# Optimization experiments

Hardware: AMD Instinct MI355X
Metric: run time of the kernel (lower is better)

Reference implementation:

```python
import math
import jax, jax.numpy as jnp
import numpy as np


def _unskew(X):
    # X: B x M x (M+L)  ->  B x M x L (each row i shifted left by i)
    B, M, MpL = X.shape
    L = MpL - M
    X = X.reshape(B, M * MpL)
    X = jnp.pad(X, ((0, 0), (0, M)))          # B x (M*(M+L)+M)
    X = X.reshape(B, M, MpL + 1)               # B x M x (M+L+1)
    return X[:, :, :L]


def _skew(X, pad_value):
    # X: B x M x L  ->  B x M x (M+L) (each row i shifted right by i)
    B, M, L = X.shape
    X = jnp.pad(X, ((0, 0), (0, 0), (0, M + 1)), constant_values=pad_value)
    X = X.reshape(B, -1)[:, :-M]               # B x (M*(M+L))
    return X.reshape(B, M, M + L)


def setup_inputs() -> dict:
    key = jax.random.key(0)
    k1, k2, k3, k4 = jax.random.split(key, 4)
    B, M, L, H = 128, 512, 1024, 64   # B = batch*heads, key len = M+L
    query = jax.random.normal(k1, (B, M, H), dtype=jnp.float32)
    key_t = jax.random.normal(k2, (B, M + L, H), dtype=jnp.float32)
    value = jax.random.normal(k3, (B, M + L, H), dtype=jnp.float32)
    key_pe = jax.random.normal(k4, (1, H, L), dtype=jnp.float32) * 0.02
    return {"query": query, "key": key_t, "value": value, "key_pe": key_pe}


def reference(query, key, value, key_pe):
    H = query.shape[-1]  # head_dim
    # content attention: B x M x (M+L), then unskew to relative coords B x M x L
    attn_cont = jnp.einsum('bmh,bnh->bmn', query, key)
    attn_cont = _unskew(attn_cont)
    # position attention: B x M x L (key_pe broadcasts over batch)
    attn_pos = jnp.einsum('bmh,xhl->bml', query, key_pe)
    attn = (attn_cont + attn_pos) / math.sqrt(H)
    attn = jax.nn.softmax(attn, axis=-1)
    # dropout p=0.0 -> identity
    attn_sk = _skew(attn, 0.0)                  # B x M x (M+L)
    out = jnp.einsum('bmn,bnh->bmh', attn_sk, value)
    return out
```

## Files before the change

kernel.cpp:

```cpp
#include <hip/hip_runtime.h>
#include <math.h>

typedef __bf16 bf16x8 __attribute__((ext_vector_type(8)));
typedef __bf16 bf16x4 __attribute__((ext_vector_type(4)));
typedef float  f32x4  __attribute__((ext_vector_type(4)));

constexpr int B_  = 128;
constexpr int M_  = 512;
constexpr int L_  = 1024;
constexpr int H_  = 64;
constexpr int KL_ = 1536;

constexpr int BM = 64;
constexpr int KT = 64;
constexpr int NT = 17;
constexpr int KS = 72;
constexpr int PPS = 256;
constexpr int PSS = 40;

constexpr int OFF_KS   = 0;
constexpr int OFF_VT   = 18432;
constexpr int OFF_PPOS = 36864;
constexpr int OFF_PS   = 69632;
constexpr int SMEM_BYTES = 79872;
constexpr int OFF_OBUF = 0;
constexpr int OFF_LSUM = 18432;
constexpr int OBS = 36;

#define MFMA16(A, B, C) __builtin_amdgcn_mfma_f32_16x16x32_bf16((A), (B), (C), 0, 0, 0)

__global__ __launch_bounds__(256, 2)
void seqattn_v5(const float* __restrict__ Q, const float* __restrict__ K,
                const float* __restrict__ V, const float* __restrict__ PE,
                float* __restrict__ O) {
  __shared__ alignas(16) char smem[SMEM_BYTES];
  __bf16* ksb  = (__bf16*)(smem + OFF_KS);
  __bf16* vtb  = (__bf16*)(smem + OFF_VT);
  __bf16* ppos = (__bf16*)(smem + OFF_PPOS);

  const int tid  = threadIdx.x;
  const int w    = tid >> 6;
  const int lane = tid & 63;
  const int nid  = lane & 15;
  const int qid  = lane >> 4;
  const int a    = w >> 1;
  const int c    = w & 1;
  const int b    = blockIdx.x;
  const int m0   = blockIdx.y * BM;
  const int swz  = qid << 4;

  __bf16* ps = (__bf16*)(smem + OFF_PS) + w * 32 * PSS;

  bf16x8 aq[2][2];
  #pragma unroll
  for (int it = 0; it < 2; ++it) {
    const float* qg = &Q[((size_t)b * M_ + m0 + 32 * a + 16 * it + nid) * H_];
    #pragma unroll
    for (int j = 0; j < 8; ++j) {
      aq[it][0][j] = (__bf16)qg[8 * qid + j];
      aq[it][1][j] = (__bf16)qg[32 + 8 * qid + j];
    }
  }

  f32x4 o[2][4];
  float lpart[2][4];
  #pragma unroll
  for (int it = 0; it < 2; ++it) {
    #pragma unroll
    for (int ht = 0; ht < 4; ++ht) o[it][ht] = (f32x4){0.f, 0.f, 0.f, 0.f};
    #pragma unroll
    for (int r = 0; r < 4; ++r) lpart[it][r] = 0.f;
  }

  const int krow = tid >> 2,  khq = (tid & 3) * 16;
  const int vj = (tid & 15) * 4, vh = (tid >> 4) * 4;

  const float* peg = &PE[(size_t)(8 * qid) * L_ + 32 * c + nid];

  f32x4 kr[4], vr[4];
  {
    const float* kg = &K[((size_t)b * KL_ + m0 + krow) * H_ + khq];
    kr[0] = *(const f32x4*)kg;       kr[1] = *(const f32x4*)(kg + 4);
    kr[2] = *(const f32x4*)(kg + 8); kr[3] = *(const f32x4*)(kg + 12);
    const float* vg = &V[((size_t)b * KL_ + m0 + vj) * H_ + vh];
    #pragma unroll
    for (int e = 0; e < 4; ++e) vr[e] = *(const f32x4*)(vg + e * H_);
  }
  {
    const f32x4 z = {0.f, 0.f, 0.f, 0.f};
    #pragma unroll
    for (int nt = 0; nt < 2; ++nt) {
      bf16x8 b0, b1;
      #pragma unroll
      for (int j = 0; j < 8; ++j) {
        b0[j] = (__bf16)peg[(size_t)j * L_ + 16 * nt];
        b1[j] = (__bf16)peg[(size_t)(32 + j) * L_ + 16 * nt];
      }
      const int colb = 32 * c + 16 * nt + nid;
      #pragma unroll
      for (int it = 0; it < 2; ++it) {
        f32x4 pp = MFMA16(aq[it][0], b0, z);
        pp = MFMA16(aq[it][1], b1, pp);
        #pragma unroll
        for (int r = 0; r < 4; ++r)
          ppos[(32 * a + 16 * it + 4 * qid + r) * PPS + (colb ^ swz)] = (__bf16)pp[r];
      }
    }
  }
  {
    bf16x8 x0, x1;
    #pragma unroll
    for (int j = 0; j < 4; ++j) {
      x0[j] = (__bf16)kr[0][j]; x0[4 + j] = (__bf16)kr[1][j];
      x1[j] = (__bf16)kr[2][j]; x1[4 + j] = (__bf16)kr[3][j];
    }
    *(bf16x8*)&ksb[krow * KS + khq] = x0;
    *(bf16x8*)&ksb[krow * KS + khq + 8] = x1;
    #pragma unroll
    for (int e = 0; e < 4; ++e) {
      bf16x4 y = {(__bf16)vr[0][e], (__bf16)vr[1][e], (__bf16)vr[2][e], (__bf16)vr[3][e]};
      *(bf16x4*)&vtb[(vh + e) * KS + vj] = y;
    }
  }
  __syncthreads();

  for (int t = 0; t < NT; ++t) {
    if (t < 16) {
      const int j1 = m0 + KT * (t + 1);
      const float* kg = &K[((size_t)b * KL_ + j1 + krow) * H_ + khq];
      kr[0] = *(const f32x4*)kg;       kr[1] = *(const f32x4*)(kg + 4);
      kr[2] = *(const f32x4*)(kg + 8); kr[3] = *(const f32x4*)(kg + 12);
      const float* vg = &V[((size_t)b * KL_ + j1 + vj) * H_ + vh];
      #pragma unroll
      for (int e = 0; e < 4; ++e) vr[e] = *(const f32x4*)(vg + e * H_);
    }
    bf16x8 pf[2][2];
    const int ch = t + 1;
    if (t < 15) {
      const float* pc = peg + ch * 64;
      #pragma unroll
      for (int nt = 0; nt < 2; ++nt) {
        #pragma unroll
        for (int j = 0; j < 8; ++j) {
          pf[nt][0][j] = (__bf16)pc[(size_t)j * L_ + 16 * nt];
          pf[nt][1][j] = (__bf16)pc[(size_t)(32 + j) * L_ + 16 * nt];
        }
      }
    }

    const __bf16* kst = ksb + (t & 1) * 64 * KS;
    const __bf16* vtt = vtb + (t & 1) * 64 * KS;
    const f32x4 z = {0.f, 0.f, 0.f, 0.f};

    f32x4 s[2][2];
    #pragma unroll
    for (int nt = 0; nt < 2; ++nt) {
      const __bf16* kb = &kst[(32 * c + 16 * nt + nid) * KS];
      const bf16x8 b0 = *(const bf16x8*)&kb[8 * qid];
      const bf16x8 b1 = *(const bf16x8*)&kb[32 + 8 * qid];
      #pragma unroll
      for (int it = 0; it < 2; ++it) {
        s[it][nt] = MFMA16(aq[it][0], b0, z);
        s[it][nt] = MFMA16(aq[it][1], b1, s[it][nt]);
      }
    }

    if (t < 15) {
      #pragma unroll
      for (int nt = 0; nt < 2; ++nt) {
        const int colb = ((ch & 3) << 6) + 32 * c + 16 * nt + nid;
        #pragma unroll
        for (int it = 0; it < 2; ++it) {
          f32x4 pp = MFMA16(aq[it][0], pf[nt][0], z);
          pp = MFMA16(aq[it][1], pf[nt][1], pp);
          #pragma unroll
          for (int r = 0; r < 4; ++r)
            ppos[(32 * a + 16 * it + 4 * qid + r) * PPS + (colb ^ swz)] = (__bf16)pp[r];
        }
      }
    }

    const bool edge = (t == 0) || (t == 16);
    #pragma unroll
    for (int it = 0; it < 2; ++it) {
      #pragma unroll
      for (int r = 0; r < 4; ++r) {
        const int il = 32 * a + 16 * it + 4 * qid + r;
        const int rb = il * PPS;
        #pragma unroll
        for (int nt = 0; nt < 2; ++nt) {
          const int l = KT * t + 32 * c + 16 * nt + nid - il;
          float p;
          if (!edge || (unsigned)l < 1024u) {
            const float pe = (float)ppos[rb + ((l & 255) ^ swz)];
            p = __expf((s[it][nt][r] + pe) * 0.125f);
          } else {
            p = 0.f;
          }
          lpart[it][r] += p;
          ps[(16 * it + 4 * qid + r) * PSS + 16 * nt + nid] = (__bf16)p;
        }
      }
    }

    #pragma unroll
    for (int it = 0; it < 2; ++it) {
      const bf16x8 ap = *(const bf16x8*)&ps[(16 * it + nid) * PSS + 8 * qid];
      #pragma unroll
      for (int ht = 0; ht < 4; ++ht) {
        o[it][ht] = MFMA16(ap, *(const bf16x8*)&vtt[(16 * ht + nid) * KS + 32 * c + 8 * qid],
                           o[it][ht]);
      }
    }

    if (t < 16) {
      __bf16* ksn = ksb + ((t + 1) & 1) * 64 * KS;
      __bf16* vtn = vtb + ((t + 1) & 1) * 64 * KS;
      bf16x8 x0, x1;
      #pragma unroll
      for (int j = 0; j < 4; ++j) {
        x0[j] = (__bf16)kr[0][j]; x0[4 + j] = (__bf16)kr[1][j];
        x1[j] = (__bf16)kr[2][j]; x1[4 + j] = (__bf16)kr[3][j];
      }
      *(bf16x8*)&ksn[krow * KS + khq] = x0;
      *(bf16x8*)&ksn[krow * KS + khq + 8] = x1;
      #pragma unroll
      for (int e = 0; e < 4; ++e) {
        bf16x4 y = {(__bf16)vr[0][e], (__bf16)vr[1][e], (__bf16)vr[2][e], (__bf16)vr[3][e]};
        *(bf16x4*)&vtn[(vh + e) * KS + vj] = y;
      }
    }
    __syncthreads();
  }

  float* lsum = (float*)(smem + OFF_LSUM);
  float* obuf = (float*)(smem + OFF_OBUF);

  #pragma unroll
  for (int it = 0; it < 2; ++it) {
    #pragma unroll
    for (int r = 0; r < 4; ++r) {
      float v = lpart[it][r];
      v += __shfl_xor(v, 1); v += __shfl_xor(v, 2);
      v += __shfl_xor(v, 4); v += __shfl_xor(v, 8);
      lpart[it][r] = v;
    }
  }
  if (nid == 0) {
    #pragma unroll
    for (int it = 0; it < 2; ++it)
      #pragma unroll
      for (int r = 0; r < 4; ++r)
        lsum[c * 64 + 32 * a + 16 * it + 4 * qid + r] = lpart[it][r];
  }
  if (c == 1) {
    #pragma unroll
    for (int it = 0; it < 2; ++it)
      #pragma unroll
      for (int ht = 0; ht < 4; ++ht)
        *(f32x4*)&obuf[(a * 64 + 16 * ht + nid) * OBS + 16 * it + 4 * qid] = o[it][ht];
  }
  __syncthreads();
  if (c == 0) {
    float inv[2][4];
    #pragma unroll
    for (int it = 0; it < 2; ++it)
      #pragma unroll
      for (int r = 0; r < 4; ++r) {
        const int row = 32 * a + 16 * it + 4 * qid + r;
        inv[it][r] = 1.f / (lsum[row] + lsum[64 + row]);
      }
    #pragma unroll
    for (int it = 0; it < 2; ++it) {
      #pragma unroll
      for (int ht = 0; ht < 4; ++ht) {
        f32x4 oo = o[it][ht] +
                   *(const f32x4*)&obuf[(a * 64 + 16 * ht + nid) * OBS + 16 * it + 4 * qid];
        #pragma unroll
        for (int r = 0; r < 4; ++r) {
          const int row = 32 * a + 16 * it + 4 * qid + r;
          O[((size_t)b * M_ + m0 + row) * H_ + 16 * ht + nid] = oo[r] * inv[it][r];
        }
      }
    }
  }
}

extern "C" void kernel_launch(void* const* d_in, const int* in_sizes, int n_in,
                              void* d_out, int out_size, void* d_ws, size_t ws_size,
                              hipStream_t stream) {
  const float* Q  = (const float*)d_in[0];
  const float* K  = (const float*)d_in[1];
  const float* V  = (const float*)d_in[2];
  const float* PE = (const float*)d_in[3];
  float* O = (float*)d_out;

  dim3 grid(B_, M_ / BM);
  hipLaunchKernelGGL(seqattn_v5, grid, dim3(256), 0, stream, Q, K, V, PE, O);
}
```

Baseline: 222.4 us.

## Shrink shared memory to single-buffer K/V and 3-slot position ring for 3 blocks/CU

Replaces the double-buffered K/V tiles with single buffers and an extra barrier, and shrinks the position-score buffer from a 4-slot to a 3-slot ring. This cuts LDS per block so three blocks fit per CU instead of two. It also folds the 1/sqrt(H)·log2(e) factor into Q so the softmax uses exp2 with no per-element multiply. The trade-off is a second __syncthreads per tile and tighter register limits, which may cause spills.

Result: slower. 309.7 us (+39.3%).

```diff
diff --git a/kernel.cpp b/kernel.cpp
--- a/kernel.cpp
+++ b/kernel.cpp
@@ -15,27 +15,29 @@
 constexpr int KT = 64;
 constexpr int NT = 17;
 constexpr int KS = 72;
-constexpr int PPS = 256;
+constexpr int PPS = 192;
 constexpr int PSS = 40;
 
 constexpr int OFF_KS   = 0;
-constexpr int OFF_VT   = 18432;
-constexpr int OFF_PPOS = 36864;
-constexpr int OFF_PS   = 69632;
-constexpr int SMEM_BYTES = 79872;
+constexpr int OFF_VT   = 9216;
+constexpr int OFF_PPOS = 18432;
+constexpr int OFF_PS   = 43008;
+constexpr int SMEM_BYTES = 53248;
 constexpr int OFF_OBUF = 0;
 constexpr int OFF_LSUM = 18432;
 constexpr int OBS = 36;
 
+constexpr float QSCALE = 0.18033688011112043f;
+
 #define MFMA16(A, B, C) __builtin_amdgcn_mfma_f32_16x16x32_bf16((A), (B), (C), 0, 0, 0)
 
-__global__ __launch_bounds__(256, 2)
-void seqattn_v5(const float* __restrict__ Q, const float* __restrict__ K,
+__global__ __launch_bounds__(256, 3)
+void seqattn_v6(const float* __restrict__ Q, const float* __restrict__ K,
                 const float* __restrict__ V, const float* __restrict__ PE,
                 float* __restrict__ O) {
   __shared__ alignas(16) char smem[SMEM_BYTES];
-  __bf16* ksb  = (__bf16*)(smem + OFF_KS);
-  __bf16* vtb  = (__bf16*)(smem + OFF_VT);
+  __bf16* ks   = (__bf16*)(smem + OFF_KS);
+  __bf16* vt   = (__bf16*)(smem + OFF_VT);
   __bf16* ppos = (__bf16*)(smem + OFF_PPOS);
 
   const int tid  = threadIdx.x;
@@ -57,8 +59,8 @@
     const float* qg = &Q[((size_t)b * M_ + m0 + 32 * a + 16 * it + nid) * H_];
     #pragma unroll
     for (int j = 0; j < 8; ++j) {
-      aq[it][0][j] = (__bf16)qg[8 * qid + j];
-      aq[it][1][j] = (__bf16)qg[32 + 8 * qid + j];
+      aq[it][0][j] = (__bf16)(qg[8 * qid + j] * QSCALE);
+      aq[it][1][j] = (__bf16)(qg[32 + 8 * qid + j] * QSCALE);
     }
   }
 
@@ -77,14 +79,26 @@
 
   const float* peg = &PE[(size_t)(8 * qid) * L_ + 32 * c + nid];
 
-  f32x4 kr[4], vr[4];
   {
     const float* kg = &K[((size_t)b * KL_ + m0 + krow) * H_ + khq];
-    kr[0] = *(const f32x4*)kg;       kr[1] = *(const f32x4*)(kg + 4);
-    kr[2] = *(const f32x4*)(kg + 8); kr[3] = *(const f32x4*)(kg + 12);
+    f32x4 k0 = *(const f32x4*)kg,       k1 = *(const f32x4*)(kg + 4);
+    f32x4 k2 = *(const f32x4*)(kg + 8), k3 = *(const f32x4*)(kg + 12);
     const float* vg = &V[((size_t)b * KL_ + m0 + vj) * H_ + vh];
-    #pragma unroll
-    for (int e = 0; e < 4; ++e) vr[e] = *(const f32x4*)(vg + e * H_);
+    f32x4 v0 = *(const f32x4*)vg,          v1 = *(const f32x4*)(vg + H_);
+    f32x4 v2 = *(const f32x4*)(vg + 2*H_), v3 = *(const f32x4*)(vg + 3*H_);
+    bf16x8 x0, x1;
+    #pragma unroll
+    for (int j = 0; j < 4; ++j) {
+      x0[j] = (__bf16)k0[j]; x0[4 + j] = (__bf16)k1[j];
+      x1[j] = (__bf16)k2[j]; x1[4 + j] = (__bf16)k3[j];
+    }
+    *(bf16x8*)&ks[krow * KS + khq] = x0;
+    *(bf16x8*)&ks[krow * KS + khq + 8] = x1;
+    #pragma unroll
+    for (int e = 0; e < 4; ++e) {
+      bf16x4 y = {(__bf16)v0[e], (__bf16)v1[e], (__bf16)v2[e], (__bf16)v3[e]};
+      *(bf16x4*)&vt[(vh + e) * KS + vj] = y;
+    }
   }
   {
     const f32x4 z = {0.f, 0.f, 0.f, 0.f};
@@ -96,35 +110,21 @@
         b0[j] = (__bf16)peg[(size_t)j * L_ + 16 * nt];
         b1[j] = (__bf16)peg[(size_t)(32 + j) * L_ + 16 * nt];
       }
-      const int colb = 32 * c + 16 * nt + nid;
+      const int colb = (32 * c + 16 * nt + nid) ^ swz;
       #pragma unroll
       for (int it = 0; it < 2; ++it) {
         f32x4 pp = MFMA16(aq[it][0], b0, z);
         pp = MFMA16(aq[it][1], b1, pp);
         #pragma unroll
         for (int r = 0; r < 4; ++r)
-          ppos[(32 * a + 16 * it + 4 * qid + r) * PPS + (colb ^ swz)] = (__bf16)pp[r];
-      }
-    }
-  }
-  {
-    bf16x8 x0, x1;
-    #pragma unroll
-    for (int j = 0; j < 4; ++j) {
-      x0[j] = (__bf16)kr[0][j]; x0[4 + j] = (__bf16)kr[1][j];
-      x1[j] = (__bf16)kr[2][j]; x1[4 + j] = (__bf16)kr[3][j];
-    }
-    *(bf16x8*)&ksb[krow * KS + khq] = x0;
-    *(bf16x8*)&ksb[krow * KS + khq + 8] = x1;
-    #pragma unroll
-    for (int e = 0; e < 4; ++e) {
-      bf16x4 y = {(__bf16)vr[0][e], (__bf16)vr[1][e], (__bf16)vr[2][e], (__bf16)vr[3][e]};
-      *(bf16x4*)&vtb[(vh + e) * KS + vj] = y;
+          ppos[(32 * a + 16 * it + 4 * qid + r) * PPS + colb] = (__bf16)pp[r];
+      }
     }
   }
   __syncthreads();
 
   for (int t = 0; t < NT; ++t) {
+    f32x4 kr[4], vr[4];
     if (t < 16) {
       const int j1 = m0 + KT * (t + 1);
       const float* kg = &K[((size_t)b * KL_ + j1 + krow) * H_ + khq];
@@ -148,14 +148,12 @@
       }
     }
 
-    const __bf16* kst = ksb + (t & 1) * 64 * KS;
-    const __bf16* vtt = vtb + (t & 1) * 64 * KS;
     const f32x4 z = {0.f, 0.f, 0.f, 0.f};
 
     f32x4 s[2][2];
     #pragma unroll
     for (int nt = 0; nt < 2; ++nt) {
-      const __bf16* kb = &kst[(32 * c + 16 * nt + nid) * KS];
+      const __bf16* kb = &ks[(32 * c + 16 * nt + nid) * KS];
       const bf16x8 b0 = *(const bf16x8*)&kb[8 * qid];
       const bf16x8 b1 = *(const bf16x8*)&kb[32 + 8 * qid];
       #pragma unroll
@@ -166,21 +164,24 @@
     }
 
     if (t < 15) {
+      const int sb = 64 * ((t + 1) % 3);
       #pragma unroll
       for (int nt = 0; nt < 2; ++nt) {
-        const int colb = ((ch & 3) << 6) + 32 * c + 16 * nt + nid;
+        const int colb = sb + ((32 * c + 16 * nt + nid) ^ swz);
         #pragma unroll
         for (int it = 0; it < 2; ++it) {
           f32x4 pp = MFMA16(aq[it][0], pf[nt][0], z);
           pp = MFMA16(aq[it][1], pf[nt][1], pp);
           #pragma unroll
           for (int r = 0; r < 4; ++r)
-            ppos[(32 * a + 16 * it + 4 * qid + r) * PPS + (colb ^ swz)] = (__bf16)pp[r];
+            ppos[(32 * a + 16 * it + 4 * qid + r) * PPS + colb] = (__bf16)pp[r];
         }
       }
     }
 
     const bool edge = (t == 0) || (t == 16);
+    const int bc = 64 * (t % 3);
+    const int bp = 64 * ((t + 2) % 3);
     #pragma unroll
     for (int it = 0; it < 2; ++it) {
       #pragma unroll
@@ -189,11 +190,13 @@
         const int rb = il * PPS;
         #pragma unroll
         for (int nt = 0; nt < 2; ++nt) {
-          const int l = KT * t + 32 * c + 16 * nt + nid - il;
+          const int delta = 32 * c + 16 * nt + nid - il;
+          const int l = KT * t + delta;
           float p;
           if (!edge || (unsigned)l < 1024u) {
-            const float pe = (float)ppos[rb + ((l & 255) ^ swz)];
-            p = __expf((s[it][nt][r] + pe) * 0.125f);
+            const int col = (delta < 0 ? bp : bc) + ((delta & 63) ^ swz);
+            const float pe = (float)ppos[rb + col];
+            p = exp2f(s[it][nt][r] + pe);
           } else {
             p = 0.f;
           }
@@ -208,26 +211,26 @@
       const bf16x8 ap = *(const bf16x8*)&ps[(16 * it + nid) * PSS + 8 * qid];
       #pragma unroll
       for (int ht = 0; ht < 4; ++ht) {
-        o[it][ht] = MFMA16(ap, *(const bf16x8*)&vtt[(16 * ht + nid) * KS + 32 * c + 8 * qid],
+        o[it][ht] = MFMA16(ap, *(const bf16x8*)&vt[(16 * ht + nid) * KS + 32 * c + 8 * qid],
                            o[it][ht]);
       }
     }
 
+    __syncthreads();
+
     if (t < 16) {
-      __bf16* ksn = ksb + ((t + 1) & 1) * 64 * KS;
-      __bf16* vtn = vtb + ((t + 1) & 1) * 64 * KS;
       bf16x8 x0, x1;
       #pragma unroll
       for (int j = 0; j < 4; ++j) {
         x0[j] = (__bf16)kr[0][j]; x0[4 + j] = (__bf16)kr[1][j];
         x1[j] = (__bf16)kr[2][j]; x1[4 + j] = (__bf16)kr[3][j];
       }
-      *(bf16x8*)&ksn[krow * KS + khq] = x0;
-      *(bf16x8*)&ksn[krow * KS + khq + 8] = x1;
+      *(bf16x8*)&ks[krow * KS + khq] = x0;
+      *(bf16x8*)&ks[krow * KS + khq + 8] = x1;
       #pragma unroll
       for (int e = 0; e < 4; ++e) {
         bf16x4 y = {(__bf16)vr[0][e], (__bf16)vr[1][e], (__bf16)vr[2][e], (__bf16)vr[3][e]};
-        *(bf16x4*)&vtn[(vh + e) * KS + vj] = y;
+        *(bf16x4*)&vt[(vh + e) * KS + vj] = y;
       }
     }
     __syncthreads();
@@ -296,5 +299,5 @@
   float* O = (float*)d_out;
 
   dim3 grid(B_, M_ / BM);
-  hipLaunchKernelGGL(seqattn_v5, grid, dim3(256), 0, stream, Q, K, V, PE, O);
+  hipLaunchKernelGGL(seqattn_v6, grid, dim3(256), 0, stream, Q, K, V, PE, O);
 }
```
